# Performance work log

Measured on AMD Instinct MI355X. Metric: run time of the kernel, lower is better.

The kernel has to match this reference:

```python
import jax, jax.numpy as jnp
import numpy as np

B, G, CIN, COUT = 1024, 64, 512, 512  # G = s**(num_layers-1) = 2**6


def setup_inputs() -> dict:
    key = jax.random.key(0)
    kx, kw = jax.random.split(key)
    x = jax.random.normal(kx, (B, G, CIN), dtype=jnp.float32)
    weight = jax.random.normal(kw, (G, CIN, COUT), dtype=jnp.float32)
    return {"x": x, "weight": weight}


def reference(x, weight):
    # Original: (x[:,:,:,None] * W[None]).sum(2) / sqrt(Cin), then sum over groups.
    # Fused equivalent: grouped contraction over (g, c) -> [B, Cout].
    scale = 1.0 / jnp.sqrt(jnp.asarray(x.shape[2], dtype=x.dtype))
    out = jnp.einsum("bgc,gco->bo", x, weight) * scale
    return out
```

## Files before the change

### kernel.cpp

```cpp
#include <hip/hip_runtime.h>
#include <hip/hip_bf16.h>

typedef __bf16 bf16x8 __attribute__((ext_vector_type(8)));
typedef __bf16 bf16x4 __attribute__((ext_vector_type(4)));
typedef float  f32x4  __attribute__((ext_vector_type(4)));

#define B_SZ    1024
#define COUT_SZ 512
#define K_SZ    32768
#define TM 128
#define TN 128
#define BK 32
#define APITCH 36
#define WPAN (COUT_SZ * BK)

__device__ __forceinline__ void async_copy16(const void* g, void* l) {
  __builtin_amdgcn_global_load_lds(
      (const __attribute__((address_space(1))) unsigned int*)g,
      (__attribute__((address_space(3))) unsigned int*)l, 16, 0, 0);
}

__device__ __forceinline__ void block_barrier() {
  __builtin_amdgcn_sched_barrier(0);
  asm volatile("" ::: "memory");
  __builtin_amdgcn_s_barrier();
  asm volatile("" ::: "memory");
  __builtin_amdgcn_sched_barrier(0);
}

__global__ __launch_bounds__(256) void wtrans_kernel(
    const float* __restrict__ w, __bf16* __restrict__ wt) {
  __shared__ float t[64 * 65];
  const int kb = (blockIdx.x & 511) * 64;
  const int ob = (blockIdx.x >> 9) * 64;
  const int tid = threadIdx.x;
  {
    const int o4 = (tid & 15) * 4;
    const int kr = tid >> 4;
    const float* src = w + (size_t)(kb + kr) * COUT_SZ + ob + o4;
#pragma unroll
    for (int i = 0; i < 4; ++i) {
      f32x4 v = *(const f32x4*)(src + (size_t)(16 * i) * COUT_SZ);
      *(f32x4*)&t[(kr + 16 * i) * 65 + o4] = v;
    }
  }
  __syncthreads();
  {
    const int orow = tid >> 3;
    const int k8   = (tid & 7) * 8;
#pragma unroll
    for (int j = 0; j < 2; ++j) {
      const int o = orow + 32 * j;
      bf16x8 pk;
#pragma unroll
      for (int e = 0; e < 8; ++e) pk[e] = (__bf16)t[(k8 + e) * 65 + o];
      *(bf16x8*)(wt + (size_t)((kb + k8) >> 5) * WPAN
                 + (size_t)(ob + o) * BK + (k8 & 31)) = pk;
    }
  }
}

__global__ __launch_bounds__(256, 4)
void gemm_kernel(const float* __restrict__ x, const __bf16* __restrict__ wt,
                 __bf16* __restrict__ dst, int kchunk, int S) {
  __shared__ __bf16 As[2][TM * APITCH];
  __shared__ __bf16 Bs[2][TN * BK];

  const int lin = blockIdx.x;
  const int z = lin % S;
  const int t = lin / S;
  const int m0 = (t & 7) * TM;
  const int n0 = (t >> 3) * TN;
  const int tid  = threadIdx.x;
  const int w    = tid >> 6;
  const int lane = tid & 63;
  const int kbase = z * kchunk;

  const int ar = tid >> 1;
  const int ah = tid & 1;
  const float* ag = x + (size_t)(m0 + ar) * K_SZ + kbase + ah * 16;
  const int awOff = ar * APITCH + ah * 16;

  const int sRow = lane >> 2;
  const int sCh  = (lane & 3) ^ (sRow & 3);
  const __bf16* bg0 = wt + (size_t)(kbase >> 5) * WPAN
                    + (size_t)(n0 + w * 32 + sRow) * BK + sCh * 8;
  const __bf16* bg1 = bg0 + 16 * BK;
  const int bL0 = (w * 32) * BK;
  const int bL1 = bL0 + 16 * BK;

  const int lm = lane & 15;
  const int q  = lane >> 4;
  const int wm = (w & 1) * 64;
  const int wn = (w >> 1) * 64;
  const int pc = q ^ (lm & 3);

  f32x4 acc[4][4];
#pragma unroll
  for (int i = 0; i < 4; ++i)
#pragma unroll
    for (int j = 0; j < 4; ++j)
      acc[i][j] = (f32x4){0.f, 0.f, 0.f, 0.f};

  f32x4 pa0 = *(const f32x4*)(ag);
  f32x4 pa1 = *(const f32x4*)(ag + 4);
  f32x4 pa2 = *(const f32x4*)(ag + 8);
  f32x4 pa3 = *(const f32x4*)(ag + 12);
  ag += BK;
  async_copy16(bg0, &Bs[0][bL0]);
  async_copy16(bg1, &Bs[0][bL1]);
  bg0 += WPAN; bg1 += WPAN;

  const int niter = kchunk / BK;
  for (int it = 0; it < niter; ++it) {
    const int cur = it & 1;
    {
      __bf16* aw = &As[cur][awOff];
      bf16x4 c0, c1, c2, c3;
#pragma unroll
      for (int e = 0; e < 4; ++e) {
        c0[e] = (__bf16)pa0[e]; c1[e] = (__bf16)pa1[e];
        c2[e] = (__bf16)pa2[e]; c3[e] = (__bf16)pa3[e];
      }
      *(bf16x4*)(aw)      = c0;
      *(bf16x4*)(aw + 4)  = c1;
      *(bf16x4*)(aw + 8)  = c2;
      *(bf16x4*)(aw + 12) = c3;
    }
    if (it + 1 < niter) {
      pa0 = *(const f32x4*)(ag);
      pa1 = *(const f32x4*)(ag + 4);
      pa2 = *(const f32x4*)(ag + 8);
      pa3 = *(const f32x4*)(ag + 12);
      ag += BK;
      const int nxt = cur ^ 1;
      async_copy16(bg0, &Bs[nxt][bL0]);
      async_copy16(bg1, &Bs[nxt][bL1]);
      bg0 += WPAN; bg1 += WPAN;
      asm volatile("s_waitcnt vmcnt(6) lgkmcnt(0)" ::: "memory");
    } else {
      asm volatile("s_waitcnt vmcnt(0) lgkmcnt(0)" ::: "memory");
    }
    block_barrier();

    bf16x8 af[4];
#pragma unroll
    for (int i = 0; i < 4; ++i) {
      const __bf16* arow = &As[cur][(wm + i * 16 + lm) * APITCH + q * 8];
      bf16x4 lo = *(const bf16x4*)arow;
      bf16x4 hi = *(const bf16x4*)(arow + 4);
      bf16x8 a;
#pragma unroll
      for (int e = 0; e < 4; ++e) { a[e] = lo[e]; a[e + 4] = hi[e]; }
      af[i] = a;
    }
    __builtin_amdgcn_s_setprio(1);
#pragma unroll
    for (int j = 0; j < 4; ++j) {
      bf16x8 bfr = *(const bf16x8*)&Bs[cur][(wn + j * 16 + lm) * BK + pc * 8];
#pragma unroll
      for (int i = 0; i < 4; ++i)
        acc[i][j] = __builtin_amdgcn_mfma_f32_16x16x32_bf16(af[i], bfr,
                                                            acc[i][j], 0, 0, 0);
    }
    __builtin_amdgcn_s_setprio(0);
    block_barrier();
  }

  __bf16* outp = dst + (size_t)z * (B_SZ * COUT_SZ)
               + (size_t)(m0 + wm + q * 4) * COUT_SZ + (n0 + wn + lm);
#pragma unroll
  for (int i = 0; i < 4; ++i) {
#pragma unroll
    for (int r = 0; r < 4; ++r) {
      __bf16* o2 = outp + (size_t)(i * 16 + r) * COUT_SZ;
#pragma unroll
      for (int j = 0; j < 4; ++j)
        o2[j * 16] = (__bf16)acc[i][j][r];
    }
  }
}

__global__ __launch_bounds__(256) void reduce_kernel(
    const __bf16* __restrict__ p, float* __restrict__ out, int S, float scale) {
  const size_t i = ((size_t)blockIdx.x * 256 + threadIdx.x) * 4;
  float s0 = 0.f, s1 = 0.f, s2 = 0.f, s3 = 0.f;
#pragma unroll 4
  for (int zz = 0; zz < S; ++zz) {
    bf16x4 v = *(const bf16x4*)(p + (size_t)zz * (B_SZ * COUT_SZ) + i);
    s0 += (float)v[0]; s1 += (float)v[1];
    s2 += (float)v[2]; s3 += (float)v[3];
  }
  f32x4 o = {s0 * scale, s1 * scale, s2 * scale, s3 * scale};
  *(f32x4*)(out + i) = o;
}

extern "C" void kernel_launch(void* const* d_in, const int* in_sizes, int n_in,
                              void* d_out, int out_size, void* d_ws, size_t ws_size,
                              hipStream_t stream) {
  const float* x = (const float*)d_in[0];
  const float* w = (const float*)d_in[1];
  float* out = (float*)d_out;

  const size_t wtB    = (size_t)COUT_SZ * K_SZ * sizeof(__bf16);
  const size_t sliceB = (size_t)B_SZ * COUT_SZ * sizeof(__bf16);

  __bf16* wt = (__bf16*)d_ws;
  __bf16* partials = (__bf16*)((char*)d_ws + wtB);

  int S = 32;
  while (S > 1 && wtB + (size_t)S * sliceB > ws_size) S >>= 1;

  const float scale = 0.04419417382415922f;

  hipLaunchKernelGGL(wtrans_kernel, dim3((K_SZ / 64) * (COUT_SZ / 64)), dim3(256),
                     0, stream, w, wt);
  hipLaunchKernelGGL(gemm_kernel, dim3(32 * S), dim3(256), 0, stream,
                     x, wt, partials, K_SZ / S, S);
  hipLaunchKernelGGL(reduce_kernel, dim3(B_SZ * COUT_SZ / (256 * 4)), dim3(256),
                     0, stream, partials, out, S, scale);
}
```

Baseline: 286.7 us.

## Pre-convert x to bf16 and stream A tiles via async LDS DMA

Adds a prep pass that converts x from fp32 to bf16 in the workspace, fused into one launch with the weight transpose. When the workspace is large enough, the GEMM then loads A tiles with global_load_lds async copies instead of register loads plus in-loop conversion. This removes the per-iteration VALU conversion and the LDS stores from the main loop, and the old padded A pitch and B swizzle are dropped. In exchange it adds a full extra read and write of x (about 64MB of fp32 read and 64MB of bf16 written), and the unpadded, unswizzled LDS layout may cause bank conflicts on fragment reads.

```diff
diff --git a/kernel.cpp b/kernel.cpp
--- a/kernel.cpp
+++ b/kernel.cpp
@@ -11,7 +11,6 @@
 #define TM 128
 #define TN 128
 #define BK 32
-#define APITCH 36
 #define WPAN (COUT_SZ * BK)
 
 __device__ __forceinline__ void async_copy16(const void* g, void* l) {
@@ -28,11 +27,29 @@
   __builtin_amdgcn_sched_barrier(0);
 }
 
-__global__ __launch_bounds__(256) void wtrans_kernel(
+__global__ __launch_bounds__(256) void prep_kernel(
+    const float* __restrict__ x, __bf16* __restrict__ xb,
     const float* __restrict__ w, __bf16* __restrict__ wt) {
   __shared__ float t[64 * 65];
-  const int kb = (blockIdx.x & 511) * 64;
-  const int ob = (blockIdx.x >> 9) * 64;
+  if (blockIdx.x < 8192) {
+    if (xb == nullptr) return;
+    const int lane = threadIdx.x & 63;
+    const int wv   = threadIdx.x >> 6;
+    const size_t base = (size_t)blockIdx.x * 4096 + wv * 1024 + lane * 4;
+#pragma unroll
+    for (int i = 0; i < 4; ++i) {
+      const size_t off = base + i * 256;
+      f32x4 v = *(const f32x4*)(x + off);
+      bf16x4 c;
+#pragma unroll
+      for (int e = 0; e < 4; ++e) c[e] = (__bf16)v[e];
+      *(bf16x4*)(xb + off) = c;
+    }
+    return;
+  }
+  const int bid = blockIdx.x - 8192;
+  const int kb = (bid & 511) * 64;
+  const int ob = (bid >> 9) * 64;
   const int tid = threadIdx.x;
   {
     const int o4 = (tid & 15) * 4;
@@ -60,10 +77,12 @@
   }
 }
 
+template <bool DMA_A>
 __global__ __launch_bounds__(256, 4)
-void gemm_kernel(const float* __restrict__ x, const __bf16* __restrict__ wt,
-                 __bf16* __restrict__ dst, int kchunk, int S) {
-  __shared__ __bf16 As[2][TM * APITCH];
+void gemm_t(const float* __restrict__ xf, const __bf16* __restrict__ xb,
+            const __bf16* __restrict__ wt, __bf16* __restrict__ dst,
+            int kchunk, int S) {
+  __shared__ __bf16 As[2][TM * BK];
   __shared__ __bf16 Bs[2][TN * BK];
 
   const int lin = blockIdx.x;
@@ -76,45 +95,50 @@
   const int lane = tid & 63;
   const int kbase = z * kchunk;
 
+  const int sR = lane >> 2;
+  const int sC = lane & 3;
+  const __bf16* ag0 = xb + (size_t)(m0 + w * 32 + sR) * K_SZ + kbase + sC * 8;
+  const __bf16* ag1 = ag0 + (size_t)16 * K_SZ;
   const int ar = tid >> 1;
   const int ah = tid & 1;
-  const float* ag = x + (size_t)(m0 + ar) * K_SZ + kbase + ah * 16;
-  const int awOff = ar * APITCH + ah * 16;
-
-  const int sRow = lane >> 2;
-  const int sCh  = (lane & 3) ^ (sRow & 3);
+  const float* agf = xf + (size_t)(m0 + ar) * K_SZ + kbase + ah * 16;
+  const int awOff = ar * BK + ah * 16;
   const __bf16* bg0 = wt + (size_t)(kbase >> 5) * WPAN
-                    + (size_t)(n0 + w * 32 + sRow) * BK + sCh * 8;
+                    + (size_t)(n0 + w * 32 + sR) * BK + sC * 8;
   const __bf16* bg1 = bg0 + 16 * BK;
-  const int bL0 = (w * 32) * BK;
-  const int bL1 = bL0 + 16 * BK;
+  const int L0 = (w * 32) * BK, L1 = L0 + 16 * BK;
 
   const int lm = lane & 15;
   const int q  = lane >> 4;
   const int wm = (w & 1) * 64;
   const int wn = (w >> 1) * 64;
-  const int pc = q ^ (lm & 3);
 
   f32x4 acc[4][4];
 #pragma unroll
   for (int i = 0; i < 4; ++i)
 #pragma unroll
-    for (int j = 0; j < 4; ++j)
-      acc[i][j] = (f32x4){0.f, 0.f, 0.f, 0.f};
-
-  f32x4 pa0 = *(const f32x4*)(ag);
-  f32x4 pa1 = *(const f32x4*)(ag + 4);
-  f32x4 pa2 = *(const f32x4*)(ag + 8);
-  f32x4 pa3 = *(const f32x4*)(ag + 12);
-  ag += BK;
-  async_copy16(bg0, &Bs[0][bL0]);
-  async_copy16(bg1, &Bs[0][bL1]);
+    for (int j = 0; j < 4; ++j) acc[i][j] = (f32x4){0.f, 0.f, 0.f, 0.f};
+
+  f32x4 pa0, pa1, pa2, pa3;
+  if constexpr (DMA_A) {
+    async_copy16(ag0, &As[0][L0]);
+    async_copy16(ag1, &As[0][L1]);
+    ag0 += BK; ag1 += BK;
+  } else {
+    pa0 = *(const f32x4*)(agf);
+    pa1 = *(const f32x4*)(agf + 4);
+    pa2 = *(const f32x4*)(agf + 8);
+    pa3 = *(const f32x4*)(agf + 12);
+    agf += BK;
+  }
+  async_copy16(bg0, &Bs[0][L0]);
+  async_copy16(bg1, &Bs[0][L1]);
   bg0 += WPAN; bg1 += WPAN;
 
   const int niter = kchunk / BK;
   for (int it = 0; it < niter; ++it) {
     const int cur = it & 1;
-    {
+    if constexpr (!DMA_A) {
       __bf16* aw = &As[cur][awOff];
       bf16x4 c0, c1, c2, c3;
 #pragma unroll
@@ -122,22 +146,29 @@
         c0[e] = (__bf16)pa0[e]; c1[e] = (__bf16)pa1[e];
         c2[e] = (__bf16)pa2[e]; c3[e] = (__bf16)pa3[e];
       }
-      *(bf16x4*)(aw)      = c0;
-      *(bf16x4*)(aw + 4)  = c1;
-      *(bf16x4*)(aw + 8)  = c2;
-      *(bf16x4*)(aw + 12) = c3;
+      *(bf16x4*)(aw) = c0; *(bf16x4*)(aw + 4) = c1;
+      *(bf16x4*)(aw + 8) = c2; *(bf16x4*)(aw + 12) = c3;
     }
     if (it + 1 < niter) {
-      pa0 = *(const f32x4*)(ag);
-      pa1 = *(const f32x4*)(ag + 4);
-      pa2 = *(const f32x4*)(ag + 8);
-      pa3 = *(const f32x4*)(ag + 12);
-      ag += BK;
       const int nxt = cur ^ 1;
-      async_copy16(bg0, &Bs[nxt][bL0]);
-      async_copy16(bg1, &Bs[nxt][bL1]);
+      if constexpr (DMA_A) {
+        async_copy16(ag0, &As[nxt][L0]);
+        async_copy16(ag1, &As[nxt][L1]);
+        ag0 += BK; ag1 += BK;
+      } else {
+        pa0 = *(const f32x4*)(agf);
+        pa1 = *(const f32x4*)(agf + 4);
+        pa2 = *(const f32x4*)(agf + 8);
+        pa3 = *(const f32x4*)(agf + 12);
+        agf += BK;
+      }
+      async_copy16(bg0, &Bs[nxt][L0]);
+      async_copy16(bg1, &Bs[nxt][L1]);
       bg0 += WPAN; bg1 += WPAN;
-      asm volatile("s_waitcnt vmcnt(6) lgkmcnt(0)" ::: "memory");
+      if constexpr (DMA_A)
+        asm volatile("s_waitcnt vmcnt(4)" ::: "memory");
+      else
+        asm volatile("s_waitcnt vmcnt(6) lgkmcnt(0)" ::: "memory");
     } else {
       asm volatile("s_waitcnt vmcnt(0) lgkmcnt(0)" ::: "memory");
     }
@@ -145,19 +176,12 @@
 
     bf16x8 af[4];
 #pragma unroll
-    for (int i = 0; i < 4; ++i) {
-      const __bf16* arow = &As[cur][(wm + i * 16 + lm) * APITCH + q * 8];
-      bf16x4 lo = *(const bf16x4*)arow;
-      bf16x4 hi = *(const bf16x4*)(arow + 4);
-      bf16x8 a;
-#pragma unroll
-      for (int e = 0; e < 4; ++e) { a[e] = lo[e]; a[e + 4] = hi[e]; }
-      af[i] = a;
-    }
+    for (int i = 0; i < 4; ++i)
+      af[i] = *(const bf16x8*)&As[cur][(wm + i * 16 + lm) * BK + q * 8];
     __builtin_amdgcn_s_setprio(1);
 #pragma unroll
     for (int j = 0; j < 4; ++j) {
-      bf16x8 bfr = *(const bf16x8*)&Bs[cur][(wn + j * 16 + lm) * BK + pc * 8];
+      bf16x8 bfr = *(const bf16x8*)&Bs[cur][(wn + j * 16 + lm) * BK + q * 8];
 #pragma unroll
       for (int i = 0; i < 4; ++i)
         acc[i][j] = __builtin_amdgcn_mfma_f32_16x16x32_bf16(af[i], bfr,
@@ -175,8 +199,7 @@
     for (int r = 0; r < 4; ++r) {
       __bf16* o2 = outp + (size_t)(i * 16 + r) * COUT_SZ;
 #pragma unroll
-      for (int j = 0; j < 4; ++j)
-        o2[j * 16] = (__bf16)acc[i][j][r];
+      for (int j = 0; j < 4; ++j) o2[j * 16] = (__bf16)acc[i][j][r];
     }
   }
 }
@@ -202,21 +225,35 @@
   const float* w = (const float*)d_in[1];
   float* out = (float*)d_out;
 
+  const size_t xbB    = (size_t)B_SZ * K_SZ * sizeof(__bf16);
   const size_t wtB    = (size_t)COUT_SZ * K_SZ * sizeof(__bf16);
   const size_t sliceB = (size_t)B_SZ * COUT_SZ * sizeof(__bf16);
-
-  __bf16* wt = (__bf16*)d_ws;
-  __bf16* partials = (__bf16*)((char*)d_ws + wtB);
-
-  int S = 32;
-  while (S > 1 && wtB + (size_t)S * sliceB > ws_size) S >>= 1;
-
   const float scale = 0.04419417382415922f;
 
-  hipLaunchKernelGGL(wtrans_kernel, dim3((K_SZ / 64) * (COUT_SZ / 64)), dim3(256),
-                     0, stream, w, wt);
-  hipLaunchKernelGGL(gemm_kernel, dim3(32 * S), dim3(256), 0, stream,
-                     x, wt, partials, K_SZ / S, S);
-  hipLaunchKernelGGL(reduce_kernel, dim3(B_SZ * COUT_SZ / (256 * 4)), dim3(256),
-                     0, stream, partials, out, S, scale);
-}
+  const bool use_xb = (xbB + wtB + sliceB) <= ws_size;
+
+  if (use_xb) {
+    __bf16* xb = (__bf16*)d_ws;
+    __bf16* wt = (__bf16*)((char*)d_ws + xbB);
+    __bf16* partials = (__bf16*)((char*)d_ws + xbB + wtB);
+    int S = 32;
+    while (S > 1 && xbB + wtB + (size_t)S * sliceB > ws_size) S >>= 1;
+    hipLaunchKernelGGL(prep_kernel, dim3(12288), dim3(256), 0, stream,
+                       x, xb, w, wt);
+    hipLaunchKernelGGL((gemm_t<true>), dim3(32 * S), dim3(256), 0, stream,
+                       x, xb, wt, partials, K_SZ / S, S);
+    hipLaunchKernelGGL(reduce_kernel, dim3(B_SZ * COUT_SZ / (256 * 4)),
+                       dim3(256), 0, stream, partials, out, S, scale);
+  } else {
+    __bf16* wt = (__bf16*)d_ws;
+    __bf16* partials = (__bf16*)((char*)d_ws + wtB);
+    int S = 32;
+    while (S > 1 && wtB + (size_t)S * sliceB > ws_size) S >>= 1;
+    hipLaunchKernelGGL(prep_kernel, dim3(12288), dim3(256), 0, stream,
+                       x, (__bf16*)nullptr, w, wt);
+    hipLaunchKernelGGL((gemm_t<false>), dim3(32 * S), dim3(256), 0, stream,
+                       x, (const __bf16*)nullptr, wt, partials, K_SZ / S, S);
+    hipLaunchKernelGGL(reduce_kernel, dim3(B_SZ * COUT_SZ / (256 * 4)),
+                       dim3(256), 0, stream, partials, out, S, scale);
+  }
+}
```

Result: slower. 302.0 us (+5.3%).

## Restructure GEMM main loop to stage next A tile during current compute

Applied to the files above, without the earlier changes.

The main loop now converts and writes the next A tile to LDS and issues the next B async copies after the top barrier, while the current fragments are being read. This is meant to overlap the fp32-to-bf16 staging with MFMA work. The XOR swizzle on the B tile in LDS is removed, which may bring back LDS bank conflicts. A full vmcnt(0) wait now happens each iteration, which may expose global-load latency. The reduce loop unroll is also raised from 4 to 8.

```diff
diff --git a/kernel.cpp b/kernel.cpp
--- a/kernel.cpp
+++ b/kernel.cpp
@@ -28,7 +28,7 @@
   __builtin_amdgcn_sched_barrier(0);
 }
 
-__global__ __launch_bounds__(256) void wtrans_kernel(
+__global__ __launch_bounds__(256) void prep_kernel(
     const float* __restrict__ w, __bf16* __restrict__ wt) {
   __shared__ float t[64 * 65];
   const int kb = (blockIdx.x & 511) * 64;
@@ -60,6 +60,20 @@
   }
 }
 
+__device__ __forceinline__ void stageA(__bf16* aw, f32x4 p0, f32x4 p1,
+                                       f32x4 p2, f32x4 p3) {
+  bf16x4 c0, c1, c2, c3;
+#pragma unroll
+  for (int e = 0; e < 4; ++e) {
+    c0[e] = (__bf16)p0[e]; c1[e] = (__bf16)p1[e];
+    c2[e] = (__bf16)p2[e]; c3[e] = (__bf16)p3[e];
+  }
+  *(bf16x4*)(aw)      = c0;
+  *(bf16x4*)(aw + 4)  = c1;
+  *(bf16x4*)(aw + 8)  = c2;
+  *(bf16x4*)(aw + 12) = c3;
+}
+
 __global__ __launch_bounds__(256, 4)
 void gemm_kernel(const float* __restrict__ x, const __bf16* __restrict__ wt,
                  __bf16* __restrict__ dst, int kchunk, int S) {
@@ -80,84 +94,78 @@
   const int ah = tid & 1;
   const float* ag = x + (size_t)(m0 + ar) * K_SZ + kbase + ah * 16;
   const int awOff = ar * APITCH + ah * 16;
-
-  const int sRow = lane >> 2;
-  const int sCh  = (lane & 3) ^ (sRow & 3);
+  const int sR = lane >> 2;
+  const int sC = lane & 3;
   const __bf16* bg0 = wt + (size_t)(kbase >> 5) * WPAN
-                    + (size_t)(n0 + w * 32 + sRow) * BK + sCh * 8;
+                    + (size_t)(n0 + w * 32 + sR) * BK + sC * 8;
   const __bf16* bg1 = bg0 + 16 * BK;
-  const int bL0 = (w * 32) * BK;
-  const int bL1 = bL0 + 16 * BK;
+  const int L0 = (w * 32) * BK, L1 = L0 + 16 * BK;
 
   const int lm = lane & 15;
   const int q  = lane >> 4;
   const int wm = (w & 1) * 64;
   const int wn = (w >> 1) * 64;
-  const int pc = q ^ (lm & 3);
 
   f32x4 acc[4][4];
 #pragma unroll
   for (int i = 0; i < 4; ++i)
 #pragma unroll
-    for (int j = 0; j < 4; ++j)
-      acc[i][j] = (f32x4){0.f, 0.f, 0.f, 0.f};
+    for (int j = 0; j < 4; ++j) acc[i][j] = (f32x4){0.f, 0.f, 0.f, 0.f};
 
   f32x4 pa0 = *(const f32x4*)(ag);
   f32x4 pa1 = *(const f32x4*)(ag + 4);
   f32x4 pa2 = *(const f32x4*)(ag + 8);
   f32x4 pa3 = *(const f32x4*)(ag + 12);
   ag += BK;
-  async_copy16(bg0, &Bs[0][bL0]);
-  async_copy16(bg1, &Bs[0][bL1]);
+  async_copy16(bg0, &Bs[0][L0]);
+  async_copy16(bg1, &Bs[0][L1]);
   bg0 += WPAN; bg1 += WPAN;
+  stageA(&As[0][awOff], pa0, pa1, pa2, pa3);
+  pa0 = *(const f32x4*)(ag);
+  pa1 = *(const f32x4*)(ag + 4);
+  pa2 = *(const f32x4*)(ag + 8);
+  pa3 = *(const f32x4*)(ag + 12);
+  ag += BK;
 
   const int niter = kchunk / BK;
   for (int it = 0; it < niter; ++it) {
     const int cur = it & 1;
-    {
-      __bf16* aw = &As[cur][awOff];
-      bf16x4 c0, c1, c2, c3;
-#pragma unroll
-      for (int e = 0; e < 4; ++e) {
-        c0[e] = (__bf16)pa0[e]; c1[e] = (__bf16)pa1[e];
-        c2[e] = (__bf16)pa2[e]; c3[e] = (__bf16)pa3[e];
-      }
-      *(bf16x4*)(aw)      = c0;
-      *(bf16x4*)(aw + 4)  = c1;
-      *(bf16x4*)(aw + 8)  = c2;
-      *(bf16x4*)(aw + 12) = c3;
-    }
+    const int nxt = cur ^ 1;
+    asm volatile("s_waitcnt vmcnt(0) lgkmcnt(0)" ::: "memory");
+    block_barrier();
+
     if (it + 1 < niter) {
+      async_copy16(bg0, &Bs[nxt][L0]);
+      async_copy16(bg1, &Bs[nxt][L1]);
+      bg0 += WPAN; bg1 += WPAN;
+    }
+
+    bf16x8 af[4];
+#pragma unroll
+    for (int i = 0; i < 4; ++i) {
+      const __bf16* arow = &As[cur][(wm + i * 16 + lm) * APITCH + q * 8];
+      bf16x4 lo = *(const bf16x4*)arow;
+      bf16x4 hi = *(const bf16x4*)(arow + 4);
+      bf16x8 a;
+#pragma unroll
+      for (int e = 0; e < 4; ++e) { a[e] = lo[e]; a[e + 4] = hi[e]; }
+      af[i] = a;
+    }
+
+    if (it + 1 < niter)
+      stageA(&As[nxt][awOff], pa0, pa1, pa2, pa3);
+    if (it + 2 < niter) {
       pa0 = *(const f32x4*)(ag);
       pa1 = *(const f32x4*)(ag + 4);
       pa2 = *(const f32x4*)(ag + 8);
       pa3 = *(const f32x4*)(ag + 12);
       ag += BK;
-      const int nxt = cur ^ 1;
-      async_copy16(bg0, &Bs[nxt][bL0]);
-      async_copy16(bg1, &Bs[nxt][bL1]);
-      bg0 += WPAN; bg1 += WPAN;
-      asm volatile("s_waitcnt vmcnt(6) lgkmcnt(0)" ::: "memory");
-    } else {
-      asm volatile("s_waitcnt vmcnt(0) lgkmcnt(0)" ::: "memory");
-    }
-    block_barrier();
-
-    bf16x8 af[4];
-#pragma unroll
-    for (int i = 0; i < 4; ++i) {
-      const __bf16* arow = &As[cur][(wm + i * 16 + lm) * APITCH + q * 8];
-      bf16x4 lo = *(const bf16x4*)arow;
-      bf16x4 hi = *(const bf16x4*)(arow + 4);
-      bf16x8 a;
-#pragma unroll
-      for (int e = 0; e < 4; ++e) { a[e] = lo[e]; a[e + 4] = hi[e]; }
-      af[i] = a;
-    }
+    }
+
     __builtin_amdgcn_s_setprio(1);
 #pragma unroll
     for (int j = 0; j < 4; ++j) {
-      bf16x8 bfr = *(const bf16x8*)&Bs[cur][(wn + j * 16 + lm) * BK + pc * 8];
+      bf16x8 bfr = *(const bf16x8*)&Bs[cur][(wn + j * 16 + lm) * BK + q * 8];
 #pragma unroll
       for (int i = 0; i < 4; ++i)
         acc[i][j] = __builtin_amdgcn_mfma_f32_16x16x32_bf16(af[i], bfr,
@@ -175,8 +183,7 @@
     for (int r = 0; r < 4; ++r) {
       __bf16* o2 = outp + (size_t)(i * 16 + r) * COUT_SZ;
 #pragma unroll
-      for (int j = 0; j < 4; ++j)
-        o2[j * 16] = (__bf16)acc[i][j][r];
+      for (int j = 0; j < 4; ++j) o2[j * 16] = (__bf16)acc[i][j][r];
     }
   }
 }
@@ -185,7 +192,7 @@
     const __bf16* __restrict__ p, float* __restrict__ out, int S, float scale) {
   const size_t i = ((size_t)blockIdx.x * 256 + threadIdx.x) * 4;
   float s0 = 0.f, s1 = 0.f, s2 = 0.f, s3 = 0.f;
-#pragma unroll 4
+#pragma unroll 8
   for (int zz = 0; zz < S; ++zz) {
     bf16x4 v = *(const bf16x4*)(p + (size_t)zz * (B_SZ * COUT_SZ) + i);
     s0 += (float)v[0]; s1 += (float)v[1];
@@ -204,6 +211,7 @@
 
   const size_t wtB    = (size_t)COUT_SZ * K_SZ * sizeof(__bf16);
   const size_t sliceB = (size_t)B_SZ * COUT_SZ * sizeof(__bf16);
+  const float scale = 0.04419417382415922f;
 
   __bf16* wt = (__bf16*)d_ws;
   __bf16* partials = (__bf16*)((char*)d_ws + wtB);
@@ -211,12 +219,10 @@
   int S = 32;
   while (S > 1 && wtB + (size_t)S * sliceB > ws_size) S >>= 1;
 
-  const float scale = 0.04419417382415922f;
-
-  hipLaunchKernelGGL(wtrans_kernel, dim3((K_SZ / 64) * (COUT_SZ / 64)), dim3(256),
+  hipLaunchKernelGGL(prep_kernel, dim3((K_SZ / 64) * (COUT_SZ / 64)), dim3(256),
                      0, stream, w, wt);
   hipLaunchKernelGGL(gemm_kernel, dim3(32 * S), dim3(256), 0, stream,
                      x, wt, partials, K_SZ / S, S);
-  hipLaunchKernelGGL(reduce_kernel, dim3(B_SZ * COUT_SZ / (256 * 4)), dim3(256),
-                     0, stream, partials, out, S, scale);
-}
+  hipLaunchKernelGGL(reduce_kernel, dim3(B_SZ * COUT_SZ / (256 * 4)),
+                     dim3(256), 0, stream, partials, out, S, scale);
+}
```

Result: no change. 283.5 us (-1.1%).
